# Kernel optimization log

Measured on AMD Instinct MI355X. Metric: run time of the kernel, lower is better.

## Reference

```python
import jax, jax.numpy as jnp
import numpy as np

D_MODEL = 1024
HEADS = 16
D_K = D_MODEL // HEADS


def setup_inputs() -> dict:
    key = jax.random.key(0)
    ks = jax.random.split(key, 11)
    B, S = 4, 2048
    scale = 1.0 / np.sqrt(D_MODEL)
    return {
        "q": jax.random.normal(ks[0], (B, S, D_MODEL), jnp.float32),
        "k": jax.random.normal(ks[1], (B, S, D_MODEL), jnp.float32),
        "v": jax.random.normal(ks[2], (B, S, D_MODEL), jnp.float32),
        "wq": jax.random.normal(ks[3], (D_MODEL, D_MODEL), jnp.float32) * scale,
        "bq": jax.random.normal(ks[4], (D_MODEL,), jnp.float32) * 0.01,
        "wk": jax.random.normal(ks[5], (D_MODEL, D_MODEL), jnp.float32) * scale,
        "bk": jax.random.normal(ks[6], (D_MODEL,), jnp.float32) * 0.01,
        "wv": jax.random.normal(ks[7], (D_MODEL, D_MODEL), jnp.float32) * scale,
        "bv": jax.random.normal(ks[8], (D_MODEL,), jnp.float32) * 0.01,
        "wo": jax.random.normal(ks[9], (D_MODEL, D_MODEL), jnp.float32) * scale,
        "bo": jax.random.normal(ks[10], (D_MODEL,), jnp.float32) * 0.01,
    }


def reference(q, k, v, wq, bq, wk, bk, wv, bv, wo, bo):
    B, S, _ = q.shape
    # nn.Linear: x @ W^T + b
    qp = q @ wq.T + bq
    kp = k @ wk.T + bk
    vp = v @ wv.T + bv
    # [B, S, D] -> [B, H, S, d_k]
    def split_heads(x):
        return x.reshape(B, S, HEADS, D_K).transpose(0, 2, 1, 3)
    qh, kh, vh = split_heads(qp), split_heads(kp), split_heads(vp)
    # scaled dot-product attention (dropout p=0 -> identity)
    scores = jnp.einsum("bhsd,bhtd->bhst", qh, kh) / jnp.sqrt(jnp.float32(D_K)).astype(qh.dtype)
    attn = jax.nn.softmax(scores, axis=-1)
    ctx = jnp.einsum("bhst,bhtd->bhsd", attn, vh)
    # merge heads and output projection
    ctx = ctx.transpose(0, 2, 1, 3).reshape(B, S, D_MODEL)
    return ctx @ wo.T + bo
```

## Files before the change

kernel.cpp:

```cpp
#include <hip/hip_runtime.h>


typedef __attribute__((ext_vector_type(8))) short bf16x8;
typedef __attribute__((ext_vector_type(4))) float f32x4;
typedef unsigned int u32;

#define DEVI __device__ __forceinline__

static constexpr int S_LEN = 2048;
static constexpr int NH = 16;
static constexpr int DK = 64;
static constexpr float Q_SCALE = 0.125f * 1.44269504088896340736f;

DEVI unsigned short f2b(float f) {
    unsigned int u = __builtin_bit_cast(unsigned int, f);
    u += 0x7fffu + ((u >> 16) & 1u);
    return (unsigned short)(u >> 16);
}

DEVI u32 pkbf16(float a, float b) {
#if __has_builtin(__builtin_amdgcn_cvt_pk_bf16_f32)
    auto r = __builtin_amdgcn_cvt_pk_bf16_f32(a, b);
    return __builtin_bit_cast(u32, r);
#else
    return (u32)f2b(a) | ((u32)f2b(b) << 16);
#endif
}

DEVI f32x4 mfma16(bf16x8 a, bf16x8 b, f32x4 c) {
    return __builtin_amdgcn_mfma_f32_16x16x32_bf16(a, b, c, 0, 0, 0);
}

#define GLL16(g, l)                                                        \
    __builtin_amdgcn_global_load_lds(                                      \
        (const __attribute__((address_space(1))) u32*)(g),                 \
        (__attribute__((address_space(3))) u32*)(l), 16, 0, 0)

__global__ __launch_bounds__(256) void cvt3(
    const float* __restrict__ q, const float* __restrict__ k,
    const float* __restrict__ v, unsigned short* __restrict__ dq,
    unsigned short* __restrict__ dk, unsigned short* __restrict__ dv) {
    const int z = blockIdx.y;
    const float* src = z == 0 ? q : z == 1 ? k : v;
    unsigned short* dst = z == 0 ? dq : z == 1 ? dk : dv;
    long i = ((long)blockIdx.x * 256 + threadIdx.x) * 8;
    float4 v0 = *(const float4*)(src + i);
    float4 v1 = *(const float4*)(src + i + 4);
    uint4 o;
    o.x = pkbf16(v0.x, v0.y);
    o.y = pkbf16(v0.z, v0.w);
    o.z = pkbf16(v1.x, v1.y);
    o.w = pkbf16(v1.z, v1.w);
    *(uint4*)(dst + i) = o;
}

__global__ __launch_bounds__(256) void cvt_w(
    const float* __restrict__ a, const float* __restrict__ b,
    const float* __restrict__ c, const float* __restrict__ d,
    unsigned short* __restrict__ o) {
    const float* src = blockIdx.y == 0 ? a : blockIdx.y == 1 ? b
                     : blockIdx.y == 2 ? c : d;
    unsigned short* dst = o + (long)blockIdx.y * 1048576;
    long i = ((long)blockIdx.x * 256 + threadIdx.x) * 8;
    float4 v0 = *(const float4*)(src + i);
    float4 v1 = *(const float4*)(src + i + 4);
    uint4 ov;
    ov.x = pkbf16(v0.x, v0.y);
    ov.y = pkbf16(v0.z, v0.w);
    ov.z = pkbf16(v1.x, v1.y);
    ov.w = pkbf16(v1.z, v1.w);
    *(uint4*)(dst + i) = ov;
}

__global__ __launch_bounds__(256) void gemm_qkv(
    const unsigned short* __restrict__ aq, const unsigned short* __restrict__ ak,
    const unsigned short* __restrict__ av, const unsigned short* __restrict__ wqkv,
    const float* __restrict__ bq, const float* __restrict__ bk,
    const float* __restrict__ bv, unsigned short* __restrict__ qh,
    unsigned short* __restrict__ kh, unsigned short* __restrict__ vht) {
    __shared__ __align__(16) unsigned short As[2][128 * 32];
    __shared__ __align__(16) unsigned short Bs[2][128 * 32];
    const int tid = threadIdx.x;
    const int w = tid >> 6, l = tid & 63, l16 = l & 15, quad = l >> 4;
    const int wm = (w >> 1) * 64, wn = (w & 1) * 64;
    const int m0 = blockIdx.y * 128, n0 = blockIdx.x * 128;
    const int z = blockIdx.z;
    const unsigned short* A = z == 0 ? aq : z == 1 ? ak : av;
    const unsigned short* W = wqkv + (long)z * 1048576;
    const float* bias = z == 0 ? bq : z == 1 ? bk : bv;

    f32x4 acc[4][4] = {};

    auto stage = [&](int kt, int buf) {
        #pragma unroll
        for (int h = 0; h < 2; ++h) {
            int sb = h * 256 + w * 64;
            int slot = sb + l;
            int row = slot >> 2, c = (slot & 3) ^ ((row >> 1) & 3);
            GLL16(A + (long)(m0 + row) * 1024 + kt + c * 8, &As[buf][sb * 8]);
            GLL16(W + (long)(n0 + row) * 1024 + kt + c * 8, &Bs[buf][sb * 8]);
        }
    };

    stage(0, 0);
    __syncthreads();

    for (int ki = 0; ki < 32; ++ki) {
        if (ki < 31) stage((ki + 1) * 32, (ki + 1) & 1);
        const unsigned short* as = As[ki & 1];
        const unsigned short* bs = Bs[ki & 1];
        bf16x8 a[4], b[4];
        #pragma unroll
        for (int i = 0; i < 4; ++i) {
            int r = wm + i * 16 + l16;
            a[i] = *(const bf16x8*)(as + (r * 4 + (quad ^ ((r >> 1) & 3))) * 8);
        }
        #pragma unroll
        for (int j = 0; j < 4; ++j) {
            int r = wn + j * 16 + l16;
            b[j] = *(const bf16x8*)(bs + (r * 4 + (quad ^ ((r >> 1) & 3))) * 8);
        }
        #pragma unroll
        for (int i = 0; i < 4; ++i)
            #pragma unroll
            for (int j = 0; j < 4; ++j)
                acc[i][j] = mfma16(a[i], b[j], acc[i][j]);
        __syncthreads();
    }

    if (z < 2) {
        unsigned short* out = z == 0 ? qh : kh;
        const float scale = z == 0 ? Q_SCALE : 1.0f;
        #pragma unroll
        for (int j = 0; j < 4; ++j) {
            int n = n0 + wn + j * 16 + l16;
            float bvl = bias[n];
            int hh = n >> 6, dd = n & 63;
            #pragma unroll
            for (int i = 0; i < 4; ++i)
                #pragma unroll
                for (int r = 0; r < 4; ++r) {
                    int m = m0 + wm + i * 16 + quad * 4 + r;
                    int bb = m >> 11, ss = m & 2047;
                    out[(((long)(bb * NH + hh) * S_LEN + ss) * DK) + dd] =
                        f2b((acc[i][j][r] + bvl) * scale);
                }
        }
    } else {
        unsigned short* out = vht;
        #pragma unroll
        for (int j = 0; j < 4; ++j) {
            int n = n0 + wn + j * 16 + l16;
            float bvl = bias[n];
            int hh = n >> 6, dd = n & 63;
            #pragma unroll
            for (int i = 0; i < 4; ++i) {
                int m = m0 + wm + i * 16 + quad * 4;
                int bb = m >> 11, ss = m & 2047;
                uint2 pk;
                pk.x = pkbf16(acc[i][j][0] + bvl, acc[i][j][1] + bvl);
                pk.y = pkbf16(acc[i][j][2] + bvl, acc[i][j][3] + bvl);
                *(uint2*)(out + ((long)(bb * NH + hh) * DK + dd) * S_LEN + ss) = pk;
            }
        }
    }
}

__global__ __launch_bounds__(256) void gemm_out(
    const unsigned short* __restrict__ A, const unsigned short* __restrict__ W,
    const float* __restrict__ bias, float* __restrict__ out) {
    __shared__ __align__(16) unsigned short As[2][128 * 32];
    __shared__ __align__(16) unsigned short Bs[2][128 * 32];
    const int tid = threadIdx.x;
    const int w = tid >> 6, l = tid & 63, l16 = l & 15, quad = l >> 4;
    const int wm = (w >> 1) * 64, wn = (w & 1) * 64;
    const int m0 = blockIdx.y * 128, n0 = blockIdx.x * 128;

    f32x4 acc[4][4] = {};

    auto stage = [&](int kt, int buf) {
        #pragma unroll
        for (int h = 0; h < 2; ++h) {
            int sb = h * 256 + w * 64;
            int slot = sb + l;
            int row = slot >> 2, c = (slot & 3) ^ ((row >> 1) & 3);
            GLL16(A + (long)(m0 + row) * 1024 + kt + c * 8, &As[buf][sb * 8]);
            GLL16(W + (long)(n0 + row) * 1024 + kt + c * 8, &Bs[buf][sb * 8]);
        }
    };

    stage(0, 0);
    __syncthreads();

    for (int ki = 0; ki < 32; ++ki) {
        if (ki < 31) stage((ki + 1) * 32, (ki + 1) & 1);
        const unsigned short* as = As[ki & 1];
        const unsigned short* bs = Bs[ki & 1];
        bf16x8 a[4], b[4];
        #pragma unroll
        for (int i = 0; i < 4; ++i) {
            int r = wm + i * 16 + l16;
            a[i] = *(const bf16x8*)(as + (r * 4 + (quad ^ ((r >> 1) & 3))) * 8);
        }
        #pragma unroll
        for (int j = 0; j < 4; ++j) {
            int r = wn + j * 16 + l16;
            b[j] = *(const bf16x8*)(bs + (r * 4 + (quad ^ ((r >> 1) & 3))) * 8);
        }
        #pragma unroll
        for (int i = 0; i < 4; ++i)
            #pragma unroll
            for (int j = 0; j < 4; ++j)
                acc[i][j] = mfma16(a[i], b[j], acc[i][j]);
        __syncthreads();
    }

    #pragma unroll
    for (int j = 0; j < 4; ++j) {
        int n = n0 + wn + j * 16 + l16;
        float bv = bias[n];
        #pragma unroll
        for (int i = 0; i < 4; ++i)
            #pragma unroll
            for (int r = 0; r < 4; ++r) {
                int m = m0 + wm + i * 16 + quad * 4 + r;
                out[(long)m * 1024 + n] = acc[i][j][r] + bv;
            }
    }
}

__global__ __launch_bounds__(256, 2) void attn(
    const unsigned short* __restrict__ qh, const unsigned short* __restrict__ kh,
    const unsigned short* __restrict__ vht, unsigned short* __restrict__ ctx) {
    __shared__ __align__(16) unsigned short Kb[2][8192];
    __shared__ __align__(16) unsigned short Vb[8192];
    __shared__ __align__(16) unsigned short P[128 * 44];

    const int bh = blockIdx.y, qt = blockIdx.x, tid = threadIdx.x;
    const int w = tid >> 6, l = tid & 63, l16 = l & 15, quad = l >> 4;

    const unsigned short* kh_b = kh + (long)bh * 2048 * 64;
    const unsigned short* vh_b = vht + (long)bh * 64 * 2048;

    const unsigned short* qsrc = qh + ((long)bh * 2048 + qt * 128) * 64;
    bf16x8 qf[2][2];
    #pragma unroll
    for (int dd = 0; dd < 2; ++dd)
        #pragma unroll
        for (int i = 0; i < 2; ++i)
            qf[dd][i] = *(const bf16x8*)(qsrc + (w * 32 + i * 16 + l16) * 64 +
                                         dd * 32 + quad * 8);

    #pragma unroll
    for (int rr = 0; rr < 4; ++rr) {
        int sb = (rr * 4 + w) * 64;
        int slot = sb + l;
        int row = slot >> 3, cc = (slot & 7) ^ (row & 7);
        GLL16(kh_b + (long)row * 64 + cc * 8, &Kb[0][sb * 8]);
    }
    __syncthreads();

    f32x4 o[4][2] = {};
    float lsum[2] = {0.f, 0.f};

    for (int kt = 0; kt < 16; ++kt) {
        if (kt < 15) {
            const unsigned short* kb_g = kh_b + (long)(kt + 1) * 128 * 64;
            #pragma unroll
            for (int rr = 0; rr < 4; ++rr) {
                int sb = (rr * 4 + w) * 64;
                int slot = sb + l;
                int row = slot >> 3, cc = (slot & 7) ^ (row & 7);
                GLL16(kb_g + (long)row * 64 + cc * 8, &Kb[(kt + 1) & 1][sb * 8]);
            }
        }
        {
            const unsigned short* vb_g = vh_b + kt * 128;
            #pragma unroll
            for (int rr = 0; rr < 4; ++rr) {
                int sb = (rr * 4 + w) * 64;
                int slot = sb + l;
                int d = slot >> 4, cc = (slot & 15) ^ (d & 15);
                GLL16(vb_g + (long)d * 2048 + cc * 8, &Vb[sb * 8]);
            }
        }

        const unsigned short* kb = Kb[kt & 1];
        f32x4 sa[2][8] = {};
        #pragma unroll
        for (int dd = 0; dd < 2; ++dd) {
            bf16x8 kf[8];
            #pragma unroll
            for (int ja = 0; ja < 8; ++ja) {
                int row = ja * 16 + l16;
                kf[ja] = *(const bf16x8*)(kb + (row * 8 + ((dd * 4 + quad) ^ (row & 7))) * 8);
            }
            #pragma unroll
            for (int i = 0; i < 2; ++i)
                #pragma unroll
                for (int ja = 0; ja < 8; ++ja)
                    sa[i][ja] = mfma16(kf[ja], qf[dd][i], sa[i][ja]);
        }

        #pragma unroll
        for (int i = 0; i < 2; ++i)
            #pragma unroll
            for (int ja = 0; ja < 8; ++ja)
                #pragma unroll
                for (int r = 0; r < 4; ++r) {
                    float p = exp2f(sa[i][ja][r]);
                    sa[i][ja][r] = p;
                    lsum[i] += p;
                }

        __syncthreads();

        #pragma unroll
        for (int qtr = 0; qtr < 4; ++qtr) {
            #pragma unroll
            for (int jh = 0; jh < 2; ++jh)
                #pragma unroll
                for (int i = 0; i < 2; ++i) {
                    int row = w * 32 + i * 16 + l16;
                    int ja = qtr * 2 + jh;
                    uint2 pk;
                    pk.x = pkbf16(sa[i][ja][0], sa[i][ja][1]);
                    pk.y = pkbf16(sa[i][ja][2], sa[i][ja][3]);
                    *(uint2*)(&P[row * 44 + jh * 16 + quad * 4]) = pk;
                }
            bf16x8 vf[4], pf[2];
            #pragma unroll
            for (int jd = 0; jd < 4; ++jd) {
                int d = jd * 16 + l16;
                vf[jd] = *(const bf16x8*)(Vb + (d * 16 + ((qtr * 4 + quad) ^ l16)) * 8);
            }
            #pragma unroll
            for (int i = 0; i < 2; ++i) {
                int row = w * 32 + i * 16 + l16;
                pf[i] = *(const bf16x8*)(&P[row * 44 + quad * 8]);
            }
            #pragma unroll
            for (int jd = 0; jd < 4; ++jd)
                #pragma unroll
                for (int i = 0; i < 2; ++i)
                    o[jd][i] = mfma16(vf[jd], pf[i], o[jd][i]);
        }
        __syncthreads();
    }

    #pragma unroll
    for (int i = 0; i < 2; ++i) {
        lsum[i] += __shfl_xor(lsum[i], 16);
        lsum[i] += __shfl_xor(lsum[i], 32);
    }

    const int b = bh >> 4, hh = bh & 15;
    #pragma unroll
    for (int i = 0; i < 2; ++i) {
        float inv = 1.0f / lsum[i];
        int s = qt * 128 + w * 32 + i * 16 + l16;
        #pragma unroll
        for (int jd = 0; jd < 4; ++jd) {
            uint2 pk;
            pk.x = pkbf16(o[jd][i][0] * inv, o[jd][i][1] * inv);
            pk.y = pkbf16(o[jd][i][2] * inv, o[jd][i][3] * inv);
            *(uint2*)(&ctx[((long)(b * 2048 + s) * 1024) + hh * 64 + jd * 16 + quad * 4]) = pk;
        }
    }
}

extern "C" void kernel_launch(void* const* d_in, const int* in_sizes, int n_in,
                              void* d_out, int out_size, void* d_ws, size_t ws_size,
                              hipStream_t stream) {
    const float* q  = (const float*)d_in[0];
    const float* k  = (const float*)d_in[1];
    const float* v  = (const float*)d_in[2];
    const float* wq = (const float*)d_in[3];
    const float* bq = (const float*)d_in[4];
    const float* wk = (const float*)d_in[5];
    const float* bk = (const float*)d_in[6];
    const float* wv = (const float*)d_in[7];
    const float* bv = (const float*)d_in[8];
    const float* wo = (const float*)d_in[9];
    const float* bo = (const float*)d_in[10];
    float* out = (float*)d_out;

    const size_t NE = 8u * 1024u * 1024u;
    unsigned short* ab_q = (unsigned short*)d_ws;
    unsigned short* qh   = ab_q + NE;
    unsigned short* kh   = qh + NE;
    unsigned short* vht  = kh + NE;
    unsigned short* wb   = vht + NE;
    unsigned short* wob  = wb + 3 * 1048576;
    unsigned short* ctx  = ab_q;
    unsigned short* ab_k = (unsigned short*)d_out;
    unsigned short* ab_v = ab_k + NE;

    dim3 blk(256);
    cvt_w<<<dim3(512, 4), blk, 0, stream>>>(wq, wk, wv, wo, wb);
    cvt3<<<dim3(4096, 3), blk, 0, stream>>>(q, k, v, ab_q, ab_k, ab_v);
    gemm_qkv<<<dim3(8, 64, 3), blk, 0, stream>>>(ab_q, ab_k, ab_v, wb,
                                                 bq, bk, bv, qh, kh, vht);
    attn<<<dim3(16, 64), blk, 0, stream>>>(qh, kh, vht, ctx);
    gemm_out<<<dim3(8, 64), blk, 0, stream>>>(ctx, wob, bo, out);
}
```

Before: 419.9 us.

## Halve attention key tile to 64, raise occupancy, remap block order

Shrinks the per-iteration key/value tile in the attention kernel from 128 to 64 rows, halving LDS buffers and score registers so launch bounds can request 4 blocks per CU instead of 2. V staging swizzle is adjusted to the narrower tile, and block indices are remapped so consecutive blocks span different heads, which changes L2 locality. The loop now runs twice as many iterations with twice as many barriers and smaller global loads, trading per-iteration overhead for more latency hiding.

```diff
diff --git a/kernel.cpp b/kernel.cpp
--- a/kernel.cpp
+++ b/kernel.cpp
@@ -229,14 +229,17 @@
     }
 }
 
-__global__ __launch_bounds__(256, 2) void attn(
+__global__ __launch_bounds__(256, 4) void attn(
     const unsigned short* __restrict__ qh, const unsigned short* __restrict__ kh,
     const unsigned short* __restrict__ vht, unsigned short* __restrict__ ctx) {
-    __shared__ __align__(16) unsigned short Kb[2][8192];
-    __shared__ __align__(16) unsigned short Vb[8192];
+    __shared__ __align__(16) unsigned short Kb[2][4096];
+    __shared__ __align__(16) unsigned short Vb[4096];
     __shared__ __align__(16) unsigned short P[128 * 44];
 
-    const int bh = blockIdx.y, qt = blockIdx.x, tid = threadIdx.x;
+    const int id = blockIdx.y * 16 + blockIdx.x;
+    const int id2 = (id & 7) * 128 + (id >> 3);
+    const int qt = id2 & 15, bh = id2 >> 4;
+    const int tid = threadIdx.x;
     const int w = tid >> 6, l = tid & 63, l16 = l & 15, quad = l >> 4;
 
     const unsigned short* kh_b = kh + (long)bh * 2048 * 64;
@@ -251,61 +254,56 @@
             qf[dd][i] = *(const bf16x8*)(qsrc + (w * 32 + i * 16 + l16) * 64 +
                                          dd * 32 + quad * 8);
 
-    #pragma unroll
-    for (int rr = 0; rr < 4; ++rr) {
-        int sb = (rr * 4 + w) * 64;
-        int slot = sb + l;
-        int row = slot >> 3, cc = (slot & 7) ^ (row & 7);
-        GLL16(kh_b + (long)row * 64 + cc * 8, &Kb[0][sb * 8]);
-    }
+    auto stage_k = [&](const unsigned short* base, int buf) {
+        #pragma unroll
+        for (int rr = 0; rr < 2; ++rr) {
+            int sb = rr * 256 + w * 64;
+            int slot = sb + l;
+            int row = slot >> 3, cc = (slot & 7) ^ (row & 7);
+            GLL16(base + (long)row * 64 + cc * 8, &Kb[buf][sb * 8]);
+        }
+    };
+    auto stage_v = [&](const unsigned short* vbase) {
+        #pragma unroll
+        for (int rr = 0; rr < 2; ++rr) {
+            int sb = rr * 256 + w * 64;
+            int slot = sb + l;
+            int d = slot >> 3, cc = (slot & 7) ^ (d & 7);
+            GLL16(vbase + (long)d * 2048 + cc * 8, &Vb[sb * 8]);
+        }
+    };
+
+    stage_k(kh_b, 0);
     __syncthreads();
 
     f32x4 o[4][2] = {};
     float lsum[2] = {0.f, 0.f};
 
-    for (int kt = 0; kt < 16; ++kt) {
-        if (kt < 15) {
-            const unsigned short* kb_g = kh_b + (long)(kt + 1) * 128 * 64;
-            #pragma unroll
-            for (int rr = 0; rr < 4; ++rr) {
-                int sb = (rr * 4 + w) * 64;
-                int slot = sb + l;
-                int row = slot >> 3, cc = (slot & 7) ^ (row & 7);
-                GLL16(kb_g + (long)row * 64 + cc * 8, &Kb[(kt + 1) & 1][sb * 8]);
-            }
-        }
-        {
-            const unsigned short* vb_g = vh_b + kt * 128;
-            #pragma unroll
-            for (int rr = 0; rr < 4; ++rr) {
-                int sb = (rr * 4 + w) * 64;
-                int slot = sb + l;
-                int d = slot >> 4, cc = (slot & 15) ^ (d & 15);
-                GLL16(vb_g + (long)d * 2048 + cc * 8, &Vb[sb * 8]);
-            }
-        }
+    for (int kt = 0; kt < 32; ++kt) {
+        if (kt < 31) stage_k(kh_b + (long)(kt + 1) * 64 * 64, (kt + 1) & 1);
+        stage_v(vh_b + kt * 64);
 
         const unsigned short* kb = Kb[kt & 1];
-        f32x4 sa[2][8] = {};
+        f32x4 sa[2][4] = {};
         #pragma unroll
         for (int dd = 0; dd < 2; ++dd) {
-            bf16x8 kf[8];
-            #pragma unroll
-            for (int ja = 0; ja < 8; ++ja) {
+            bf16x8 kf[4];
+            #pragma unroll
+            for (int ja = 0; ja < 4; ++ja) {
                 int row = ja * 16 + l16;
                 kf[ja] = *(const bf16x8*)(kb + (row * 8 + ((dd * 4 + quad) ^ (row & 7))) * 8);
             }
             #pragma unroll
             for (int i = 0; i < 2; ++i)
                 #pragma unroll
-                for (int ja = 0; ja < 8; ++ja)
+                for (int ja = 0; ja < 4; ++ja)
                     sa[i][ja] = mfma16(kf[ja], qf[dd][i], sa[i][ja]);
         }
 
         #pragma unroll
         for (int i = 0; i < 2; ++i)
             #pragma unroll
-            for (int ja = 0; ja < 8; ++ja)
+            for (int ja = 0; ja < 4; ++ja)
                 #pragma unroll
                 for (int r = 0; r < 4; ++r) {
                     float p = exp2f(sa[i][ja][r]);
@@ -316,7 +314,7 @@
         __syncthreads();
 
         #pragma unroll
-        for (int qtr = 0; qtr < 4; ++qtr) {
+        for (int qtr = 0; qtr < 2; ++qtr) {
             #pragma unroll
             for (int jh = 0; jh < 2; ++jh)
                 #pragma unroll
@@ -332,7 +330,7 @@
             #pragma unroll
             for (int jd = 0; jd < 4; ++jd) {
                 int d = jd * 16 + l16;
-                vf[jd] = *(const bf16x8*)(Vb + (d * 16 + ((qtr * 4 + quad) ^ l16)) * 8);
+                vf[jd] = *(const bf16x8*)(Vb + (d * 8 + ((qtr * 4 + quad) ^ (d & 7))) * 8);
             }
             #pragma unroll
             for (int i = 0; i < 2; ++i) {
```

Measured after the change: 406.8 us. -3.1%, faster.
